# Performance work log

Hardware: AMD Instinct MI355X
Metric: run time of the kernel (lower is better)

## Reference

```python
import jax, jax.numpy as jnp
import numpy as np


def setup_inputs() -> dict:
    key = jax.random.key(0)
    kq, kk, kv, km = jax.random.split(key, 4)
    B, H, S, D = 4, 16, 2048, 64
    query = jax.random.normal(kq, (B, H, S, D), dtype=jnp.float32)
    k = jax.random.normal(kk, (B, H, S, D), dtype=jnp.float32)
    value = jax.random.normal(kv, (B, H, S, D), dtype=jnp.float32)
    mask = jax.random.randint(km, (B, S, S), 0, 2, dtype=jnp.int32)
    return {"query": query, "key": k, "value": value, "mask": mask}


def reference(query, key, value, mask):
    # query/key/value: [B, H, S, D]; mask: [B, S, S] (0 = masked out)
    d = query.shape[-1]
    scale = 1.0 / jnp.sqrt(jnp.asarray(d, dtype=query.dtype))
    scores = jnp.einsum('bhqd,bhkd->bhqk', query, key) * scale
    m = (mask[:, None, :, :] == 0)  # broadcast over heads, matches mask.unsqueeze(1).eq(0)
    min_value = jnp.finfo(scores.dtype).min
    scores = jnp.where(m, min_value, scores)
    attn = jax.nn.softmax(scores, axis=-1)
    attn = jnp.where(m, jnp.asarray(0.0, attn.dtype), attn)
    out = jnp.einsum('bhqk,bhkd->bhqd', attn, value)
    return (out, attn)
```

## Files before the change

kernel.cpp:

```cpp
#include <hip/hip_runtime.h>
#include <hip/hip_bf16.h>


typedef __attribute__((ext_vector_type(8))) short bf16x8;
typedef __attribute__((ext_vector_type(4))) short bf16x4;
typedef __attribute__((ext_vector_type(4))) float f32x4;
typedef __attribute__((ext_vector_type(4))) int i32x4;

#define MFMA32(A, B, C) __builtin_amdgcn_mfma_f32_16x16x32_bf16((A), (B), (C), 0, 0, 0)

constexpr int Bsz = 4, Hsz = 16, Ssz = 2048, Dsz = 64;
constexpr int KBLK = 64;
constexpr int NT   = Ssz / KBLK;
constexpr float SCALE = 0.125f;

static __device__ __forceinline__ short f2bf(float f) {
  __hip_bfloat16 h = __float2bfloat16(f);
  return __builtin_bit_cast(short, h);
}

static __device__ __forceinline__ void wg_barrier() {
  __builtin_amdgcn_sched_barrier(0);
  asm volatile("s_waitcnt lgkmcnt(0)" ::: "memory");
  __builtin_amdgcn_sched_barrier(0);
  __builtin_amdgcn_s_barrier();
  __builtin_amdgcn_sched_barrier(0);
}

__global__ __launch_bounds__(512, 8)
void attn_denom(const float* __restrict__ Qg, const float* __restrict__ Kg,
                const int* __restrict__ Mg, float* __restrict__ wsL,
                unsigned short* __restrict__ wsM)
{
  __shared__ short sK[2][KBLK][72];

  const int bid = blockIdx.x;
  const int lin = ((bid & 7) << 7) | (bid >> 3);
  const int bh  = lin >> 4;
  const int qt  = lin & 15;
  const int q0 = qt * 128;
  const int tid = threadIdx.x, lane = tid & 63, w = tid >> 6;
  const int lr = lane & 15, lg = lane >> 4;

  const size_t bhSD = (size_t)bh * (Ssz * Dsz);
  const float* Qb = Qg + bhSD;
  const float* Kb = Kg + bhSD;
  const int b = bh >> 4;
  const int qrow = q0 + w * 16 + lr;
  const int* Mrow = Mg + ((size_t)b * Ssz + qrow) * Ssz;
  unsigned short* wsMq = wsM + (size_t)(b * Ssz + qrow) * (NT * 4) + lg;

  bf16x8 qf[2];
  {
    const float* qp = Qb + (size_t)qrow * Dsz + lg * 8;
#pragma unroll
    for (int h = 0; h < 2; ++h) {
      f32x4 a = *(const f32x4*)(qp + h * 32);
      f32x4 c2 = *(const f32x4*)(qp + h * 32 + 4);
      bf16x8 t;
#pragma unroll
      for (int j = 0; j < 4; ++j) { t[j] = f2bf(a[j] * SCALE); t[4 + j] = f2bf(c2[j] * SCALE); }
      qf[h] = t;
    }
  }

  const int krow = tid >> 3, kd0 = (tid & 7) * 8;
  {
    const float* kp = Kb + (size_t)krow * Dsz + kd0;
    f32x4 a = *(const f32x4*)kp, c2 = *(const f32x4*)(kp + 4);
    bf16x8 t;
#pragma unroll
    for (int j = 0; j < 4; ++j) { t[j] = f2bf(a[j]); t[4 + j] = f2bf(c2[j]); }
    *(bf16x8*)(&sK[0][krow][kd0]) = t;
  }
  wg_barrier();

  float lacc = 0.f;
  for (int t = 0; t < NT; ++t) {
    const int cur = t & 1;
    f32x4 ka = {0.f,0.f,0.f,0.f}, kb2 = {0.f,0.f,0.f,0.f};
    if (t + 1 < NT) {
      const float* kp = Kb + (size_t)((t + 1) * KBLK + krow) * Dsz + kd0;
      ka  = *(const f32x4*)kp;
      kb2 = *(const f32x4*)(kp + 4);
    }
    unsigned bits = 0;
#pragma unroll
    for (int cb = 0; cb < 4; ++cb) {
      const short* kr = &sK[cur][cb * 16 + lr][0];
      bf16x8 a0 = *(const bf16x8*)(kr + lg * 8);
      bf16x8 a1 = *(const bf16x8*)(kr + 32 + lg * 8);
      f32x4 c = {0.f, 0.f, 0.f, 0.f};
      c = MFMA32(a0, qf[0], c);
      c = MFMA32(a1, qf[1], c);
      i32x4 mv = *(const i32x4*)(Mrow + t * KBLK + cb * 16 + lg * 4);
#pragma unroll
      for (int r = 0; r < 4; ++r) {
        lacc += mv[r] ? __expf(c[r]) : 0.f;
        bits |= (mv[r] ? 1u : 0u) << (cb * 4 + r);
      }
    }
    wsMq[t * 4] = (unsigned short)bits;
    if (t + 1 < NT) {
      bf16x8 t2;
#pragma unroll
      for (int j = 0; j < 4; ++j) { t2[j] = f2bf(ka[j]); t2[4 + j] = f2bf(kb2[j]); }
      *(bf16x8*)(&sK[cur ^ 1][krow][kd0]) = t2;
    }
    wg_barrier();
  }

  lacc += __shfl_xor(lacc, 16, 64);
  lacc += __shfl_xor(lacc, 32, 64);
  if (lane < 16)
    wsL[(size_t)bh * Ssz + qrow] = (lacc > 0.f) ? 1.f / lacc : 0.f;
}

__global__ __launch_bounds__(512, 8)
void attn_emit(const float* __restrict__ Qg, const float* __restrict__ Kg,
               const float* __restrict__ Vg, const float* __restrict__ wsL,
               const unsigned short* __restrict__ wsM,
               float* __restrict__ Og, float* __restrict__ Ag)
{
  __shared__ __align__(16) char smem[49152];
  auto sK  = (short(*)[KBLK][72])(smem);
  auto sVt = (short(*)[Dsz][72])(smem + 2 * 9216);
  auto sO  = (float(*)[68])(smem);

  const int bid = blockIdx.x;
  const int lin = ((bid & 7) << 8) | (bid >> 3);
  const int bh  = lin >> 5;
  const int qt  = lin & 31;
  const int q0 = qt * 64;
  const int tid = threadIdx.x, lane = tid & 63, wid = tid >> 6;
  const int wq = wid >> 1, wk = wid & 1;
  const int lr = lane & 15, lg = lane >> 4;

  const size_t bhSD = (size_t)bh * (Ssz * Dsz);
  const float* Qb = Qg + bhSD;
  const float* Kb = Kg + bhSD;
  const float* Vb = Vg + bhSD;
  const int b = bh >> 4;
  float* Ob = Og + bhSD;
  float* Ab = Ag + (size_t)bh * ((size_t)Ssz * Ssz);

  const int qrow = q0 + wq * 16 + lr;
  float* Arow = Ab + (size_t)qrow * Ssz;
  const float invl = wsL[(size_t)bh * Ssz + qrow];
  const unsigned short* wsMq = wsM + (size_t)(b * Ssz + qrow) * (NT * 4) + lg;
  const int mshift = wk * 8;

  bf16x8 qf[2];
  {
    const float* qp = Qb + (size_t)qrow * Dsz + lg * 8;
#pragma unroll
    for (int h = 0; h < 2; ++h) {
      f32x4 a = *(const f32x4*)(qp + h * 32);
      f32x4 c2 = *(const f32x4*)(qp + h * 32 + 4);
      bf16x8 t;
#pragma unroll
      for (int j = 0; j < 4; ++j) { t[j] = f2bf(a[j] * SCALE); t[4 + j] = f2bf(c2[j] * SCALE); }
      qf[h] = t;
    }
  }

  const int krow = tid >> 3;
  const int kd0  = (tid & 7) * 8;
  const int vkv  = tid & 63;
  const int vd0  = (tid >> 6) * 8;
  const int kb0  = wk * 32 + lg * 4;

  f32x4 oacc[4] = {{0,0,0,0},{0,0,0,0},{0,0,0,0},{0,0,0,0}};

  {
    const float* kp = Kb + (size_t)krow * Dsz + kd0;
    f32x4 a = *(const f32x4*)kp, c2 = *(const f32x4*)(kp + 4);
    bf16x8 t;
#pragma unroll
    for (int j = 0; j < 4; ++j) { t[j] = f2bf(a[j]); t[4 + j] = f2bf(c2[j]); }
    *(bf16x8*)(&sK[0][krow][kd0]) = t;

    const float* vp = Vb + (size_t)vkv * Dsz + vd0;
    f32x4 va = *(const f32x4*)vp, vb = *(const f32x4*)(vp + 4);
#pragma unroll
    for (int j = 0; j < 4; ++j) {
      sVt[0][vd0 + j][vkv]     = f2bf(va[j]);
      sVt[0][vd0 + 4 + j][vkv] = f2bf(vb[j]);
    }
  }
  unsigned mbn = wsMq[0];
  wg_barrier();

  for (int t = 0; t < NT; ++t) {
    const int cur = t & 1;
    const unsigned mb = mbn;
    f32x4 ka = {0.f,0.f,0.f,0.f}, kb2 = {0.f,0.f,0.f,0.f};
    f32x4 va = {0.f,0.f,0.f,0.f}, vb2 = {0.f,0.f,0.f,0.f};
    if (t + 1 < NT) {
      const float* kp = Kb + (size_t)((t + 1) * KBLK + krow) * Dsz + kd0;
      ka  = *(const f32x4*)kp;
      kb2 = *(const f32x4*)(kp + 4);
      const float* vp = Vb + (size_t)((t + 1) * KBLK + vkv) * Dsz + vd0;
      va  = *(const f32x4*)vp;
      vb2 = *(const f32x4*)(vp + 4);
      mbn  = wsMq[(t + 1) * 4];
    }
    __builtin_amdgcn_s_setprio(1);
    const short* kr0 = &sK[cur][wk * 32 + lr][0];
    const short* kr1 = &sK[cur][wk * 32 + 16 + lr][0];
    bf16x8 a00 = *(const bf16x8*)(kr0 + lg * 8);
    bf16x8 a01 = *(const bf16x8*)(kr0 + 32 + lg * 8);
    bf16x8 a10 = *(const bf16x8*)(kr1 + lg * 8);
    bf16x8 a11 = *(const bf16x8*)(kr1 + 32 + lg * 8);
    f32x4 c0 = {0.f,0.f,0.f,0.f}, c1 = {0.f,0.f,0.f,0.f};
    c0 = MFMA32(a00, qf[0], c0);
    c0 = MFMA32(a01, qf[1], c0);
    c1 = MFMA32(a10, qf[0], c1);
    c1 = MFMA32(a11, qf[1], c1);
    f32x4 p0, p1;
#pragma unroll
    for (int r = 0; r < 4; ++r) {
      p0[r] = ((mb >> (mshift + r))     & 1u) ? __expf(c0[r]) * invl : 0.f;
      p1[r] = ((mb >> (mshift + 4 + r)) & 1u) ? __expf(c1[r]) * invl : 0.f;
    }
    __builtin_nontemporal_store(p0, (f32x4*)(Arow + t * KBLK + kb0));
    __builtin_nontemporal_store(p1, (f32x4*)(Arow + t * KBLK + kb0 + 16));
    bf16x4 pf0 = {f2bf(p0[0]), f2bf(p0[1]), f2bf(p0[2]), f2bf(p0[3])};
    bf16x4 pf1 = {f2bf(p1[0]), f2bf(p1[1]), f2bf(p1[2]), f2bf(p1[3])};
    {
      bf16x4 vf0 = *(const bf16x4*)(&sVt[cur][0 * 16 + lr][wk * 32 + lg * 4]);
      bf16x4 vf1 = *(const bf16x4*)(&sVt[cur][1 * 16 + lr][wk * 32 + lg * 4]);
      bf16x4 vf2 = *(const bf16x4*)(&sVt[cur][2 * 16 + lr][wk * 32 + lg * 4]);
      bf16x4 vf3 = *(const bf16x4*)(&sVt[cur][3 * 16 + lr][wk * 32 + lg * 4]);
      asm volatile(
        "s_nop 1\n\t"
        "v_mfma_f32_16x16x16_bf16 %0, %4, %5, %0\n\t"
        "v_mfma_f32_16x16x16_bf16 %1, %4, %6, %1\n\t"
        "v_mfma_f32_16x16x16_bf16 %2, %4, %7, %2\n\t"
        "v_mfma_f32_16x16x16_bf16 %3, %4, %8, %3\n\t"
        "s_nop 2"
        : "+v"(oacc[0]), "+v"(oacc[1]), "+v"(oacc[2]), "+v"(oacc[3])
        : "v"(pf0), "v"(vf0), "v"(vf1), "v"(vf2), "v"(vf3));
    }
    {
      bf16x4 vf0 = *(const bf16x4*)(&sVt[cur][0 * 16 + lr][wk * 32 + 16 + lg * 4]);
      bf16x4 vf1 = *(const bf16x4*)(&sVt[cur][1 * 16 + lr][wk * 32 + 16 + lg * 4]);
      bf16x4 vf2 = *(const bf16x4*)(&sVt[cur][2 * 16 + lr][wk * 32 + 16 + lg * 4]);
      bf16x4 vf3 = *(const bf16x4*)(&sVt[cur][3 * 16 + lr][wk * 32 + 16 + lg * 4]);
      asm volatile(
        "s_nop 1\n\t"
        "v_mfma_f32_16x16x16_bf16 %0, %4, %5, %0\n\t"
        "v_mfma_f32_16x16x16_bf16 %1, %4, %6, %1\n\t"
        "v_mfma_f32_16x16x16_bf16 %2, %4, %7, %2\n\t"
        "v_mfma_f32_16x16x16_bf16 %3, %4, %8, %3\n\t"
        "s_nop 2"
        : "+v"(oacc[0]), "+v"(oacc[1]), "+v"(oacc[2]), "+v"(oacc[3])
        : "v"(pf1), "v"(vf0), "v"(vf1), "v"(vf2), "v"(vf3));
    }
    __builtin_amdgcn_s_setprio(0);
    if (t + 1 < NT) {
      bf16x8 t2;
#pragma unroll
      for (int j = 0; j < 4; ++j) { t2[j] = f2bf(ka[j]); t2[4 + j] = f2bf(kb2[j]); }
      *(bf16x8*)(&sK[cur ^ 1][krow][kd0]) = t2;
#pragma unroll
      for (int j = 0; j < 4; ++j) {
        sVt[cur ^ 1][vd0 + j][vkv]     = f2bf(va[j]);
        sVt[cur ^ 1][vd0 + 4 + j][vkv] = f2bf(vb2[j]);
      }
    }
    wg_barrier();
  }

  asm volatile("s_nop 7\n\ts_nop 7" :::);

  if (wk == 0) {
#pragma unroll
    for (int nb = 0; nb < 4; ++nb)
#pragma unroll
      for (int r = 0; r < 4; ++r)
        sO[wq * 16 + lg * 4 + r][nb * 16 + lr] = oacc[nb][r];
  }
  wg_barrier();
  if (wk == 1) {
#pragma unroll
    for (int nb = 0; nb < 4; ++nb)
#pragma unroll
      for (int r = 0; r < 4; ++r) {
        float v = sO[wq * 16 + lg * 4 + r][nb * 16 + lr] + oacc[nb][r];
        __builtin_nontemporal_store(v, Ob + (size_t)(q0 + wq * 16 + lg * 4 + r) * Dsz + nb * 16 + lr);
      }
  }
}

extern "C" void kernel_launch(void* const* d_in, const int* in_sizes, int n_in,
                              void* d_out, int out_size, void* d_ws, size_t ws_size,
                              hipStream_t stream) {
  const float* Q = (const float*)d_in[0];
  const float* K = (const float*)d_in[1];
  const float* V = (const float*)d_in[2];
  const int*   M = (const int*)d_in[3];
  float* Out  = (float*)d_out;
  float* Attn = Out + (size_t)Bsz * Hsz * Ssz * Dsz;
  float* wsL = (float*)d_ws;
  unsigned short* wsM = (unsigned short*)((char*)d_ws + (size_t)Bsz * Hsz * Ssz * sizeof(float));
  attn_denom<<<dim3(1024), 512, 0, stream>>>(Q, K, M, wsL, wsM);
  attn_emit <<<dim3(2048), 512, 0, stream>>>(Q, K, V, wsL, wsM, Out, Attn);
}
```

Before: 442.8 us.

## Cache bf16 exp scores in workspace instead of recomputing QK in emit pass

```diff
diff --git a/kernel.cpp b/kernel.cpp
--- a/kernel.cpp
+++ b/kernel.cpp
@@ -6,6 +6,7 @@
 typedef __attribute__((ext_vector_type(4))) short bf16x4;
 typedef __attribute__((ext_vector_type(4))) float f32x4;
 typedef __attribute__((ext_vector_type(4))) int i32x4;
+typedef __attribute__((ext_vector_type(2))) unsigned long long u64x2;
 
 #define MFMA32(A, B, C) __builtin_amdgcn_mfma_f32_16x16x32_bf16((A), (B), (C), 0, 0, 0)
 
@@ -17,6 +18,10 @@
 static __device__ __forceinline__ short f2bf(float f) {
   __hip_bfloat16 h = __float2bfloat16(f);
   return __builtin_bit_cast(short, h);
+}
+static __device__ __forceinline__ float bf2f(short s) {
+  unsigned u = ((unsigned)(unsigned short)s) << 16;
+  return __builtin_bit_cast(float, u);
 }
 
 static __device__ __forceinline__ void wg_barrier() {
@@ -26,6 +31,241 @@
   __builtin_amdgcn_s_barrier();
   __builtin_amdgcn_sched_barrier(0);
 }
+
+
+__global__ __launch_bounds__(512, 8)
+void attn_denom2(const float* __restrict__ Qg, const float* __restrict__ Kg,
+                 const int* __restrict__ Mg, float* __restrict__ wsL,
+                 unsigned long long* __restrict__ wsP)
+{
+  __shared__ short sK[2][KBLK][72];
+
+  const int bid = blockIdx.x;
+  const int lin = ((bid & 7) << 7) | (bid >> 3);
+  const int bh  = lin >> 4;
+  const int qt  = lin & 15;
+  const int q0 = qt * 128;
+  const int tid = threadIdx.x, lane = tid & 63, w = tid >> 6;
+  const int lr = lane & 15, lg = lane >> 4;
+
+  const size_t bhSD = (size_t)bh * (Ssz * Dsz);
+  const float* Qb = Qg + bhSD;
+  const float* Kb = Kg + bhSD;
+  const int b = bh >> 4;
+  const int qrow = q0 + w * 16 + lr;
+  const int* Mrow = Mg + ((size_t)b * Ssz + qrow) * Ssz;
+  unsigned long long* Prow = wsP + ((size_t)bh * Ssz + qrow) * (NT * 16) + lg * 2;
+
+  bf16x8 qf[2];
+  {
+    const float* qp = Qb + (size_t)qrow * Dsz + lg * 8;
+#pragma unroll
+    for (int h = 0; h < 2; ++h) {
+      f32x4 a = *(const f32x4*)(qp + h * 32);
+      f32x4 c2 = *(const f32x4*)(qp + h * 32 + 4);
+      bf16x8 t;
+#pragma unroll
+      for (int j = 0; j < 4; ++j) { t[j] = f2bf(a[j] * SCALE); t[4 + j] = f2bf(c2[j] * SCALE); }
+      qf[h] = t;
+    }
+  }
+
+  const int krow = tid >> 3, kd0 = (tid & 7) * 8;
+  {
+    const float* kp = Kb + (size_t)krow * Dsz + kd0;
+    f32x4 a = *(const f32x4*)kp, c2 = *(const f32x4*)(kp + 4);
+    bf16x8 t;
+#pragma unroll
+    for (int j = 0; j < 4; ++j) { t[j] = f2bf(a[j]); t[4 + j] = f2bf(c2[j]); }
+    *(bf16x8*)(&sK[0][krow][kd0]) = t;
+  }
+  wg_barrier();
+
+  float lacc = 0.f;
+  for (int t = 0; t < NT; ++t) {
+    const int cur = t & 1;
+    f32x4 ka = {0.f,0.f,0.f,0.f}, kb2 = {0.f,0.f,0.f,0.f};
+    if (t + 1 < NT) {
+      const float* kp = Kb + (size_t)((t + 1) * KBLK + krow) * Dsz + kd0;
+      ka  = *(const f32x4*)kp;
+      kb2 = *(const f32x4*)(kp + 4);
+    }
+    unsigned long long pb4_0, pb4_1, pb4_2, pb4_3;
+#pragma unroll
+    for (int cb = 0; cb < 4; ++cb) {
+      const short* kr = &sK[cur][cb * 16 + lr][0];
+      bf16x8 a0 = *(const bf16x8*)(kr + lg * 8);
+      bf16x8 a1 = *(const bf16x8*)(kr + 32 + lg * 8);
+      f32x4 c = {0.f, 0.f, 0.f, 0.f};
+      c = MFMA32(a0, qf[0], c);
+      c = MFMA32(a1, qf[1], c);
+      i32x4 mv = *(const i32x4*)(Mrow + t * KBLK + cb * 16 + lg * 4);
+      f32x4 p;
+#pragma unroll
+      for (int r = 0; r < 4; ++r) {
+        p[r] = mv[r] ? __expf(c[r]) : 0.f;
+        lacc += p[r];
+      }
+      unsigned plo = (unsigned short)f2bf(p[0]) | ((unsigned)(unsigned short)f2bf(p[1]) << 16);
+      unsigned phi = (unsigned short)f2bf(p[2]) | ((unsigned)(unsigned short)f2bf(p[3]) << 16);
+      unsigned long long pv = (unsigned long long)plo | ((unsigned long long)phi << 32);
+      if (cb == 0) pb4_0 = pv; else if (cb == 1) pb4_1 = pv;
+      else if (cb == 2) pb4_2 = pv; else pb4_3 = pv;
+    }
+    u64x2 s0 = {pb4_0, pb4_1};
+    u64x2 s1 = {pb4_2, pb4_3};
+    __builtin_nontemporal_store(s0, (u64x2*)(Prow + t * 16));
+    __builtin_nontemporal_store(s1, (u64x2*)(Prow + t * 16 + 8));
+    if (t + 1 < NT) {
+      bf16x8 t2;
+#pragma unroll
+      for (int j = 0; j < 4; ++j) { t2[j] = f2bf(ka[j]); t2[4 + j] = f2bf(kb2[j]); }
+      *(bf16x8*)(&sK[cur ^ 1][krow][kd0]) = t2;
+    }
+    wg_barrier();
+  }
+
+  lacc += __shfl_xor(lacc, 16, 64);
+  lacc += __shfl_xor(lacc, 32, 64);
+  if (lane < 16)
+    wsL[(size_t)bh * Ssz + qrow] = (lacc > 0.f) ? 1.f / lacc : 0.f;
+}
+
+__global__ __launch_bounds__(512, 8)
+void attn_emit2(const float* __restrict__ Vg, const float* __restrict__ wsL,
+                const unsigned long long* __restrict__ wsP,
+                float* __restrict__ Og, float* __restrict__ Ag)
+{
+  __shared__ __align__(16) char smem[49152];
+  auto sVt = (short(*)[Dsz][72])(smem);
+  auto sO  = (float(*)[68])(smem + 2 * 9216);
+
+  const int bid = blockIdx.x;
+  const int lin = ((bid & 7) << 8) | (bid >> 3);
+  const int bh  = lin >> 5;
+  const int qt  = lin & 31;
+  const int q0 = qt * 64;
+  const int tid = threadIdx.x, lane = tid & 63, wid = tid >> 6;
+  const int wq = wid >> 1, wk = wid & 1;
+  const int lr = lane & 15, lg = lane >> 4;
+
+  const size_t bhSD = (size_t)bh * (Ssz * Dsz);
+  const float* Vb = Vg + bhSD;
+  float* Ob = Og + bhSD;
+  float* Ab = Ag + (size_t)bh * ((size_t)Ssz * Ssz);
+
+  const int qrow = q0 + wq * 16 + lr;
+  float* Arow = Ab + (size_t)qrow * Ssz;
+  const float invl = wsL[(size_t)bh * Ssz + qrow];
+  const unsigned long long* Prow =
+      wsP + ((size_t)bh * Ssz + qrow) * (NT * 16) + wk * 8 + lg * 2;
+
+  const int vkv  = tid & 63;
+  const int vd0  = (tid >> 6) * 8;
+  const int kb0  = wk * 32 + lg * 4;
+
+  f32x4 oacc[4] = {{0,0,0,0},{0,0,0,0},{0,0,0,0},{0,0,0,0}};
+
+  {
+    const float* vp = Vb + (size_t)vkv * Dsz + vd0;
+    f32x4 va = *(const f32x4*)vp, vb = *(const f32x4*)(vp + 4);
+#pragma unroll
+    for (int j = 0; j < 4; ++j) {
+      sVt[0][vd0 + j][vkv]     = f2bf(va[j]);
+      sVt[0][vd0 + 4 + j][vkv] = f2bf(vb[j]);
+    }
+  }
+  bf16x8 pbn = *(const bf16x8*)(Prow);
+  wg_barrier();
+
+  for (int t = 0; t < NT; ++t) {
+    const int cur = t & 1;
+    const bf16x8 pb = pbn;
+    f32x4 va = {0.f,0.f,0.f,0.f}, vb2 = {0.f,0.f,0.f,0.f};
+    if (t + 1 < NT) {
+      const float* vp = Vb + (size_t)((t + 1) * KBLK + vkv) * Dsz + vd0;
+      va  = *(const f32x4*)vp;
+      vb2 = *(const f32x4*)(vp + 4);
+      pbn = *(const bf16x8*)(Prow + (size_t)(t + 1) * 16);
+    }
+    __builtin_amdgcn_s_setprio(1);
+    f32x4 p0, p1;
+#pragma unroll
+    for (int r = 0; r < 4; ++r) {
+      p0[r] = bf2f(pb[r])     * invl;
+      p1[r] = bf2f(pb[4 + r]) * invl;
+    }
+    __builtin_nontemporal_store(p0, (f32x4*)(Arow + t * KBLK + kb0));
+    __builtin_nontemporal_store(p1, (f32x4*)(Arow + t * KBLK + kb0 + 16));
+    bf16x4 pf0 = {pb[0], pb[1], pb[2], pb[3]};
+    bf16x4 pf1 = {pb[4], pb[5], pb[6], pb[7]};
+    {
+      bf16x4 vf0 = *(const bf16x4*)(&sVt[cur][0 * 16 + lr][wk * 32 + lg * 4]);
+      bf16x4 vf1 = *(const bf16x4*)(&sVt[cur][1 * 16 + lr][wk * 32 + lg * 4]);
+      bf16x4 vf2 = *(const bf16x4*)(&sVt[cur][2 * 16 + lr][wk * 32 + lg * 4]);
+      bf16x4 vf3 = *(const bf16x4*)(&sVt[cur][3 * 16 + lr][wk * 32 + lg * 4]);
+      asm volatile(
+        "s_nop 1\n\t"
+        "v_mfma_f32_16x16x16_bf16 %0, %4, %5, %0\n\t"
+        "v_mfma_f32_16x16x16_bf16 %1, %4, %6, %1\n\t"
+        "v_mfma_f32_16x16x16_bf16 %2, %4, %7, %2\n\t"
+        "v_mfma_f32_16x16x16_bf16 %3, %4, %8, %3\n\t"
+        "s_nop 2"
+        : "+v"(oacc[0]), "+v"(oacc[1]), "+v"(oacc[2]), "+v"(oacc[3])
+        : "v"(pf0), "v"(vf0), "v"(vf1), "v"(vf2), "v"(vf3));
+    }
+    {
+      bf16x4 vf0 = *(const bf16x4*)(&sVt[cur][0 * 16 + lr][wk * 32 + 16 + lg * 4]);
+      bf16x4 vf1 = *(const bf16x4*)(&sVt[cur][1 * 16 + lr][wk * 32 + 16 + lg * 4]);
+      bf16x4 vf2 = *(const bf16x4*)(&sVt[cur][2 * 16 + lr][wk * 32 + 16 + lg * 4]);
+      bf16x4 vf3 = *(const bf16x4*)(&sVt[cur][3 * 16 + lr][wk * 32 + 16 + lg * 4]);
+      asm volatile(
+        "s_nop 1\n\t"
+        "v_mfma_f32_16x16x16_bf16 %0, %4, %5, %0\n\t"
+        "v_mfma_f32_16x16x16_bf16 %1, %4, %6, %1\n\t"
+        "v_mfma_f32_16x16x16_bf16 %2, %4, %7, %2\n\t"
+        "v_mfma_f32_16x16x16_bf16 %3, %4, %8, %3\n\t"
+        "s_nop 2"
+        : "+v"(oacc[0]), "+v"(oacc[1]), "+v"(oacc[2]), "+v"(oacc[3])
+        : "v"(pf1), "v"(vf0), "v"(vf1), "v"(vf2), "v"(vf3));
+    }
+    __builtin_amdgcn_s_setprio(0);
+    if (t + 1 < NT) {
+#pragma unroll
+      for (int j = 0; j < 4; ++j) {
+        sVt[cur ^ 1][vd0 + j][vkv]     = f2bf(va[j]);
+        sVt[cur ^ 1][vd0 + 4 + j][vkv] = f2bf(vb2[j]);
+      }
+    }
+    wg_barrier();
+  }
+
+  asm volatile("s_nop 7\n\ts_nop 7" :::);
+
+  float invl4_0 = wsL[(size_t)bh * Ssz + q0 + wq * 16 + lg * 4 + 0];
+  float invl4_1 = wsL[(size_t)bh * Ssz + q0 + wq * 16 + lg * 4 + 1];
+  float invl4_2 = wsL[(size_t)bh * Ssz + q0 + wq * 16 + lg * 4 + 2];
+  float invl4_3 = wsL[(size_t)bh * Ssz + q0 + wq * 16 + lg * 4 + 3];
+  if (wk == 0) {
+#pragma unroll
+    for (int nb = 0; nb < 4; ++nb)
+#pragma unroll
+      for (int r = 0; r < 4; ++r)
+        sO[wq * 16 + lg * 4 + r][nb * 16 + lr] = oacc[nb][r];
+  }
+  wg_barrier();
+  if (wk == 1) {
+#pragma unroll
+    for (int nb = 0; nb < 4; ++nb)
+#pragma unroll
+      for (int r = 0; r < 4; ++r) {
+        float il = (r == 0) ? invl4_0 : (r == 1) ? invl4_1 : (r == 2) ? invl4_2 : invl4_3;
+        float v = (sO[wq * 16 + lg * 4 + r][nb * 16 + lr] + oacc[nb][r]) * il;
+        __builtin_nontemporal_store(v, Ob + (size_t)(q0 + wq * 16 + lg * 4 + r) * Dsz + nb * 16 + lr);
+      }
+  }
+}
+
 
 __global__ __launch_bounds__(512, 8)
 void attn_denom(const float* __restrict__ Qg, const float* __restrict__ Kg,
@@ -302,8 +542,18 @@
   const int*   M = (const int*)d_in[3];
   float* Out  = (float*)d_out;
   float* Attn = Out + (size_t)Bsz * Hsz * Ssz * Dsz;
-  float* wsL = (float*)d_ws;
-  unsigned short* wsM = (unsigned short*)((char*)d_ws + (size_t)Bsz * Hsz * Ssz * sizeof(float));
-  attn_denom<<<dim3(1024), 512, 0, stream>>>(Q, K, M, wsL, wsM);
-  attn_emit <<<dim3(2048), 512, 0, stream>>>(Q, K, V, wsL, wsM, Out, Attn);
-}
+
+  char* ws = (char*)d_ws;
+  float* wsL = (float*)ws;
+  const size_t lbytes = (size_t)Bsz * Hsz * Ssz * sizeof(float);
+  const size_t pbytes = (size_t)Bsz * Hsz * Ssz * Ssz * 2;
+  if (ws_size >= lbytes + pbytes) {
+    unsigned long long* wsP = (unsigned long long*)(ws + lbytes);
+    attn_denom2<<<dim3(1024), 512, 0, stream>>>(Q, K, M, wsL, wsP);
+    attn_emit2 <<<dim3(2048), 512, 0, stream>>>(V, wsL, wsP, Out, Attn);
+  } else {
+    unsigned short* wsM = (unsigned short*)(ws + lbytes);
+    attn_denom<<<dim3(1024), 512, 0, stream>>>(Q, K, M, wsL, wsM);
+    attn_emit <<<dim3(2048), 512, 0, stream>>>(Q, K, V, wsL, wsM, Out, Attn);
+  }
+}
```

Result: slower. 883.6 us (+99.6%).
